# Performance work log

Measured on AMD Instinct MI355X. Metric: run time of the kernel, lower is better.

Reference implementation:

```python
import jax, jax.numpy as jnp
import numpy as np

N_NODES = 100000
DROP_P = 0.1


def gcn_conv(x, W, b, row, col, n_nodes):
    """PyG GCNConv: out = D^{-1/2}(A+I)D^{-1/2} X W + b.
    row/col already include self-loops. Messages flow row(src) -> col(dst)."""
    xw = x @ W  # [N, H]
    deg = jax.ops.segment_sum(jnp.ones_like(col, dtype=xw.dtype), col, num_segments=n_nodes)
    dinv = jnp.where(deg > 0, jax.lax.rsqrt(deg), 0.0)
    norm = dinv[row] * dinv[col]  # [E]
    msg = norm[:, None] * xw[row]  # [E, H] gather + scale
    out = jax.ops.segment_sum(msg, col, num_segments=n_nodes)  # scatter-add
    return out + b


def dropout(x, key, p):
    keep = jax.random.bernoulli(key, 1.0 - p, x.shape)
    return jnp.where(keep, x / (1.0 - p), 0.0).astype(x.dtype)


def prelu(x, alpha):
    return jnp.where(x >= 0, x, alpha[None, :] * x)


def setup_inputs() -> dict:
    key = jax.random.key(0)
    k1, k2, k3, k4 = jax.random.split(key, 4)
    in_ch, hid = 128, 128
    n_edges = 1600000
    x = jax.random.normal(k1, (N_NODES, in_ch), dtype=jnp.float32)
    edge_index = jax.random.randint(k2, (2, n_edges), 0, N_NODES, dtype=jnp.int64)
    s = 1.0 / np.sqrt(in_ch)
    W1 = jax.random.normal(k3, (in_ch, hid), dtype=jnp.float32) * s
    W2 = jax.random.normal(k4, (hid, hid), dtype=jnp.float32) * s
    b1 = jnp.zeros((hid,), dtype=jnp.float32)
    b2 = jnp.zeros((hid,), dtype=jnp.float32)
    alpha = jnp.full((hid,), 0.25, dtype=jnp.float32)
    return {"x": x, "edge_index": edge_index, "W1": W1, "b1": b1,
            "W2": W2, "b2": b2, "alpha": alpha}


def reference(x, edge_index, W1, b1, W2, b2, alpha):
    n = x.shape[0]
    # add self-loops once (PyG default add_self_loops=True)
    loop = jnp.arange(n, dtype=edge_index.dtype)
    row = jnp.concatenate([edge_index[0], loop])
    col = jnp.concatenate([edge_index[1], loop])

    dk1, dk2 = jax.random.split(jax.random.key(42))
    h = gcn_conv(x, W1, b1, row, col, n)
    h = dropout(h, dk1, DROP_P)
    h = prelu(h, alpha)
    h = gcn_conv(h, W2, b2, row, col, n)
    h = dropout(h, dk2, DROP_P)
    h = prelu(h, alpha)
    return h
```

## Files before the change

kernel.cpp:

```cpp
#include <hip/hip_runtime.h>
#include <stdint.h>
#include <string.h>

__host__ __device__ inline uint32_t rotl32(uint32_t x, int r) {
    return (x << r) | (x >> (32 - r));
}

__host__ __device__ inline void tf2x32(uint32_t k0, uint32_t k1,
                                       uint32_t x0, uint32_t x1,
                                       uint32_t& o0, uint32_t& o1) {
    uint32_t ks0 = k0, ks1 = k1, ks2 = k0 ^ k1 ^ 0x1BD11BDAu;
    x0 += ks0; x1 += ks1;
#define TF_R4(a,b,c,d) \
    x0 += x1; x1 = rotl32(x1,a); x1 ^= x0; \
    x0 += x1; x1 = rotl32(x1,b); x1 ^= x0; \
    x0 += x1; x1 = rotl32(x1,c); x1 ^= x0; \
    x0 += x1; x1 = rotl32(x1,d); x1 ^= x0;
    TF_R4(13,15,26,6)  x0 += ks1; x1 += ks2 + 1u;
    TF_R4(17,29,16,24) x0 += ks2; x1 += ks0 + 2u;
    TF_R4(13,15,26,6)  x0 += ks0; x1 += ks1 + 3u;
    TF_R4(17,29,16,24) x0 += ks1; x1 += ks2 + 4u;
    TF_R4(13,15,26,6)  x0 += ks2; x1 += ks0 + 5u;
#undef TF_R4
    o0 = x0; o1 = x1;
}

__device__ inline unsigned pk2h(float a, float b) {
    _Float16 ha = (_Float16)a, hb = (_Float16)b;
    unsigned short ua, ub;
    __builtin_memcpy(&ua, &ha, 2);
    __builtin_memcpy(&ub, &hb, 2);
    return (unsigned)ua | ((unsigned)ub << 16);
}
__device__ inline unsigned short h16bits(float a) {
    _Float16 h = (_Float16)a;
    unsigned short u; __builtin_memcpy(&u, &h, 2);
    return u;
}
__device__ inline float lo16(unsigned u) {
    unsigned short s = (unsigned short)(u & 0xffffu);
    _Float16 h; __builtin_memcpy(&h, &s, 2);
    return (float)h;
}
__device__ inline float hi16(unsigned u) {
    unsigned short s = (unsigned short)(u >> 16);
    _Float16 h; __builtin_memcpy(&h, &s, 2);
    return (float)h;
}

typedef float fx4 __attribute__((ext_vector_type(4)));
typedef unsigned ux4 __attribute__((ext_vector_type(4)));
typedef _Float16 h16x8 __attribute__((ext_vector_type(8)));
typedef float f32x4 __attribute__((ext_vector_type(4)));

#define CSR_CAP 48
#define NSUP 8

__global__ __launch_bounds__(256) void k_build(
        const int* __restrict__ ei, int2* __restrict__ gsup,
        unsigned* __restrict__ gsupcnt,
        unsigned long long* __restrict__ m1, unsigned long long* __restrict__ m2,
        const float* __restrict__ x, unsigned* __restrict__ xb,
        const float* __restrict__ w1, const float* __restrict__ w2,
        _Float16* __restrict__ wt1, _Float16* __restrict__ wt2,
        unsigned k1a, unsigned k1b, unsigned k2a, unsigned k2b,
        int E, int N, int supw, int scap, int total,
        int P1A, int MB, int CB) {
    int b = blockIdx.x;
    int t = (int)threadIdx.x;
    if (b < P1A) {
        __shared__ unsigned hcnt[NSUP], hoff[NSUP], hrun[NSUP];
        if (t < NSUP) { hcnt[t] = 0; hrun[t] = 0; }
        __syncthreads();
        int e0 = b * 2048 + t;
        int r[8], c[8];
        unsigned sp[8];
#pragma unroll
        for (int i = 0; i < 8; i++) {
            int e = e0 + i * 256;
            sp[i] = 0xffu;
            if (e < E) {
                c[i] = __builtin_nontemporal_load(ei + (size_t)E + e);
                r[i] = __builtin_nontemporal_load(ei + e);
                if ((unsigned)c[i] < (unsigned)N && (unsigned)r[i] < (unsigned)N) {
                    sp[i] = (unsigned)c[i] / (unsigned)supw;
                    atomicAdd(&hcnt[sp[i]], 1u);
                }
            }
        }
        __syncthreads();
        if (t < NSUP) hoff[t] = atomicAdd(&gsupcnt[t], hcnt[t]);
        __syncthreads();
#pragma unroll
        for (int i = 0; i < 8; i++) {
            if (sp[i] < (unsigned)NSUP) {
                unsigned rank = atomicAdd(&hrun[sp[i]], 1u);
                unsigned gp = hoff[sp[i]] + rank;
                if (gp < (unsigned)scap)
                    gsup[(size_t)sp[i] * scap + gp] = make_int2(r[i], c[i]);
            }
        }
        return;
    }
    b -= P1A;
    if (b < MB) {
        int wv = (b * 256 + t) >> 6;
        int lane = t & 63;
        int TW = (2 * total) >> 6;
        int half = total >> 6;
        int w0 = wv * 8;
#pragma unroll
        for (int j = 0; j < 8; j++) {
            int wd = w0 + j;
            if (wd < TW) {
                int wl = wd;
                unsigned ka = k1a, kb = k1b;
                unsigned long long* m = m1;
                if (wl >= half) { wl -= half; ka = k2a; kb = k2b; m = m2; }
                uint32_t o0, o1;
                tf2x32(ka, kb, 0u, (uint32_t)(wl * 64 + lane), o0, o1);
                bool keep = (((o0 ^ o1) >> 9) < 7549747u);
                unsigned long long bal = __ballot(keep);
                if (lane == 0)
                    __builtin_nontemporal_store(bal, m + wl);
            }
        }
        return;
    }
    b -= MB;
    if (b < CB) {
        int i = b * 256 + t;
        if (i < (total >> 3)) {
            const fx4* src = (const fx4*)(x + (size_t)i * 8);
            fx4 a = __builtin_nontemporal_load(src);
            fx4 bb = __builtin_nontemporal_load(src + 1);
            ux4 v;
            v.x = pk2h(a.x, a.y);
            v.y = pk2h(a.z, a.w);
            v.z = pk2h(bb.x, bb.y);
            v.w = pk2h(bb.z, bb.w);
            __builtin_nontemporal_store(v, (ux4*)xb + i);
        }
        return;
    }
    b -= CB;
    int idx = b * 256 + t;
    int mat = idx >> 14;
    int e2 = idx & 16383;
    int c = e2 >> 7, k = e2 & 127;
    const float* W = mat ? w2 : w1;
    _Float16* WT = mat ? wt2 : wt1;
    WT[(size_t)c * 128 + k] = (_Float16)W[(size_t)k * 128 + c];
}

__global__ __launch_bounds__(256) void k_fill2(
        const int2* __restrict__ gsup, const unsigned* __restrict__ gsupcnt,
        unsigned* __restrict__ cnt, unsigned* __restrict__ csr, int scap) {
    int s = blockIdx.x & (NSUP - 1);
    int chunk = blockIdx.x >> 3;
    unsigned ne = gsupcnt[s];
    if (ne > (unsigned)scap) ne = (unsigned)scap;
    const int2* base = gsup + (size_t)s * scap;
    unsigned e0 = (unsigned)(chunk * 2048) + threadIdx.x;
#pragma unroll
    for (int i = 0; i < 8; i++) {
        unsigned e = e0 + i * 256;
        if (e < ne) {
            int2 ed = base[e];
            unsigned c = (unsigned)ed.y;
            unsigned slot = atomicAdd(&cnt[c], 1u);
            if (slot < (unsigned)CSR_CAP)
                csr[(size_t)c * CSR_CAP + slot] = (unsigned)ed.x;
        }
    }
}

__global__ void k_dinv(const unsigned* __restrict__ cnt, float* __restrict__ dinv, int N) {
    int n = blockIdx.x * blockDim.x + threadIdx.x;
    if (n >= N) return;
    dinv[n] = rsqrtf((float)cnt[n] + 1.0f);
}

#define UPK_FMA(c, uu)                                   \
    acc[0] = fmaf(c, lo16((uu).x), acc[0]);              \
    acc[1] = fmaf(c, hi16((uu).x), acc[1]);              \
    acc[2] = fmaf(c, lo16((uu).y), acc[2]);              \
    acc[3] = fmaf(c, hi16((uu).y), acc[3]);              \
    acc[4] = fmaf(c, lo16((uu).z), acc[4]);              \
    acc[5] = fmaf(c, hi16((uu).z), acc[5]);              \
    acc[6] = fmaf(c, lo16((uu).w), acc[6]);              \
    acc[7] = fmaf(c, hi16((uu).w), acc[7]);

template <int OUT_HALF>
__global__ __launch_bounds__(256) void k_layer(
        const unsigned short* __restrict__ in,
        const _Float16* __restrict__ WT,
        const float* __restrict__ bias, const float* __restrict__ alpha,
        const unsigned long long* __restrict__ mask,
        const float* __restrict__ dinv, const unsigned* __restrict__ cnt,
        const unsigned* __restrict__ csr,
        void* outv, int n) {
    __shared__ unsigned hl[64 * 68];
    int t = threadIdx.x;
    int rowbase = blockIdx.x * 64;
    int w = t >> 6, l = t & 63;
    int slot = l >> 4;
    int lm = l & 15;
    int ci = lm << 3;

    int prow = rowbase + w * 16 + lm;
    bool pv = prow < n;
    float dnAll = pv ? dinv[prow] : 0.f;
    unsigned cAll = pv ? cnt[prow] : 0u;
    if (cAll > (unsigned)CSR_CAP) cAll = (unsigned)CSR_CAP;

#pragma unroll
    for (int g = 0; g < 4; ++g) {
        int rloc = g * 4 + slot;
        int node = rowbase + w * 16 + rloc;
        float dn = __shfl(dnAll, rloc);
        unsigned ecnt = (unsigned)__shfl((int)cAll, rloc);
        float acc[8];
#pragma unroll
        for (int j = 0; j < 8; j++) acc[j] = 0.f;
        size_t eb = (size_t)node * CSR_CAP;
        unsigned e = 0;
        unsigned nb4 = ecnt >> 2;
#pragma unroll 2
        for (unsigned bb = 0; bb < nb4; ++bb) {
            unsigned r0 = csr[eb + e + 0];
            unsigned r1 = csr[eb + e + 1];
            unsigned r2 = csr[eb + e + 2];
            unsigned r3 = csr[eb + e + 3];
            float c0 = dn * dinv[r0];
            float c1 = dn * dinv[r1];
            float c2 = dn * dinv[r2];
            float c3 = dn * dinv[r3];
            uint4 u0 = *(const uint4*)(in + ((size_t)r0 << 7) + ci);
            uint4 u1 = *(const uint4*)(in + ((size_t)r1 << 7) + ci);
            uint4 u2 = *(const uint4*)(in + ((size_t)r2 << 7) + ci);
            uint4 u3 = *(const uint4*)(in + ((size_t)r3 << 7) + ci);
            UPK_FMA(c0, u0)
            UPK_FMA(c1, u1)
            UPK_FMA(c2, u2)
            UPK_FMA(c3, u3)
            e += 4;
        }
        for (; e < ecnt; ++e) {
            unsigned r0 = csr[eb + e];
            float c0 = dn * dinv[r0];
            uint4 u0 = *(const uint4*)(in + ((size_t)r0 << 7) + ci);
            UPK_FMA(c0, u0)
        }
        if (node < n) {
            uint4 sv = *(const uint4*)(in + ((size_t)node << 7) + ci);
            float dd = dn * dn;
            UPK_FMA(dd, sv)
        }
        uint4 o;
        o.x = pk2h(acc[0], acc[1]);
        o.y = pk2h(acc[2], acc[3]);
        o.z = pk2h(acc[4], acc[5]);
        o.w = pk2h(acc[6], acc[7]);
        *(uint4*)(hl + (size_t)(w * 16 + rloc) * 68 + lm * 4) = o;
    }

    int kq = l >> 4;
    f32x4 facc[8];
#pragma unroll
    for (int f = 0; f < 8; f++) facc[f] = (f32x4){0.f, 0.f, 0.f, 0.f};
#pragma unroll
    for (int kk = 0; kk < 4; kk++) {
        h16x8 a = *(const h16x8*)(hl + (size_t)(w * 16 + lm) * 68 + kq * 4 + kk * 16);
#pragma unroll
        for (int f = 0; f < 8; f++) {
            h16x8 bfr = *(const h16x8*)(WT + (size_t)(f * 16 + lm) * 128 + kk * 32 + kq * 8);
            facc[f] = __builtin_amdgcn_mfma_f32_16x16x32_f16(a, bfr, facc[f], 0, 0, 0);
        }
    }

#pragma unroll
    for (int j = 0; j < 4; j++) {
        int rg = rowbase + w * 16 + kq * 4 + j;
        if (rg < n) {
            unsigned long long wm0 = mask[(size_t)rg << 1];
            unsigned long long wm1 = mask[((size_t)rg << 1) + 1];
#pragma unroll
            for (int f = 0; f < 8; f++) {
                int c = f * 16 + lm;
                float v = facc[f][j] + bias[c];
                unsigned long long wmw = (f < 4) ? wm0 : wm1;
                bool keep = (wmw >> (c & 63)) & 1ull;
                v = keep ? v * (1.0f / 0.9f) : 0.0f;
                float al = alpha[c];
                v = (v >= 0.f) ? v : al * v;
                if (OUT_HALF)
                    ((unsigned short*)outv)[(size_t)rg * 128 + c] = h16bits(v);
                else
                    ((float*)outv)[(size_t)rg * 128 + c] = v;
            }
        }
    }
}

extern "C" void kernel_launch(void* const* d_in, const int* in_sizes, int n_in,
                              void* d_out, int out_size, void* d_ws, size_t ws_size,
                              hipStream_t stream) {
    const float* x  = (const float*)d_in[0];
    const int*   ei = (const int*)d_in[1];
    const float* W1 = (const float*)d_in[2];
    const float* b1 = (const float*)d_in[3];
    const float* W2 = (const float*)d_in[4];
    const float* b2 = (const float*)d_in[5];
    const float* al = (const float*)d_in[6];
    int N = in_sizes[0] / 128;
    int E = in_sizes[1] / 2;
    float* out = (float*)d_out;

    int supw = (N + NSUP - 1) / NSUP;
    int scap = E / NSUP + E / 64 + 4096;

    char* p = (char*)d_ws;
    unsigned short* xb = (unsigned short*)p;   p += (size_t)N * 128 * 2;
    unsigned short* ab = (unsigned short*)p;   p += (size_t)N * 128 * 2;
    int2* gsup = (int2*)ab;
    unsigned* cnt = (unsigned*)p;              p += (size_t)N * 4;
    float* dinv = (float*)p;                   p += (size_t)N * 4;
    unsigned* csr = (unsigned*)p;              p += (size_t)N * CSR_CAP * 4;
    unsigned long long* m1 = (unsigned long long*)p;  p += ((size_t)N * 128 / 64) * 8;
    unsigned long long* m2 = (unsigned long long*)p;  p += ((size_t)N * 128 / 64) * 8;
    _Float16* wt1 = (_Float16*)p;              p += 128 * 128 * 2;
    _Float16* wt2 = (_Float16*)p;              p += 128 * 128 * 2;
    unsigned* gsupcnt = (unsigned*)p;

    hipMemsetAsync(cnt, 0, (size_t)N * 4, stream);
    hipMemsetAsync(gsupcnt, 0, NSUP * 4, stream);

    uint32_t dk1a, dk1b, dk2a, dk2b;
    tf2x32(0u, 42u, 0u, 0u, dk1a, dk1b);
    tf2x32(0u, 42u, 0u, 1u, dk2a, dk2b);

    int total = N * 128;
    int P1A = (E + 2047) / 2048;
    int TW = (2 * total) / 64;
    int MB = (TW + 31) / 32;
    int CB = (total / 8 + 255) / 256;
    int WB = (2 * 128 * 128 + 255) / 256;
    k_build<<<P1A + MB + CB + WB, 256, 0, stream>>>(ei, gsup, gsupcnt, m1, m2,
                                                    x, (unsigned*)xb,
                                                    W1, W2, wt1, wt2,
                                                    dk1a, dk1b, dk2a, dk2b,
                                                    E, N, supw, scap, total,
                                                    P1A, MB, CB);
    int F2C = (scap + 2047) / 2048;
    k_fill2<<<NSUP * F2C, 256, 0, stream>>>(gsup, gsupcnt, cnt, csr, scap);
    k_dinv<<<(N + 255) / 256, 256, 0, stream>>>(cnt, dinv, N);

    int LB = (N + 63) / 64;
    k_layer<1><<<LB, 256, 0, stream>>>(xb, wt1, b1, al, m1, dinv, cnt, csr, ab, N);
    k_layer<0><<<LB, 256, 0, stream>>>(ab, wt2, b2, al, m2, dinv, cnt, csr, out, N);
}
```

Baseline: 371.1 us.

## Prescale features by dinv and accumulate neighbours with packed fp16 adds

The symmetric normalisation is factored so that source rows are prescaled by dinv once, in a new prep kernel for layer 1 and in the layer-1 epilogue for layer 2. The aggregation loop then drops the per-edge dinv gather and multiply and sums neighbours with packed half2 adds, applying the destination dinv once at the end. Layer blocks shrink from four wavefronts to one to raise block count. This removes a random gather per edge and halves the ALU work, but accumulating in fp16 loses precision and risks overflow at high degrees.

```diff
diff --git a/kernel.cpp b/kernel.cpp
--- a/kernel.cpp
+++ b/kernel.cpp
@@ -51,7 +51,10 @@
 typedef float fx4 __attribute__((ext_vector_type(4)));
 typedef unsigned ux4 __attribute__((ext_vector_type(4)));
 typedef _Float16 h16x8 __attribute__((ext_vector_type(8)));
+typedef _Float16 h16x2 __attribute__((ext_vector_type(2)));
 typedef float f32x4 __attribute__((ext_vector_type(4)));
+
+__device__ inline h16x2 as_h2(unsigned u) { h16x2 r; __builtin_memcpy(&r, &u, 4); return r; }
 
 #define CSR_CAP 48
 #define NSUP 8
@@ -175,24 +178,24 @@
     }
 }
 
-__global__ void k_dinv(const unsigned* __restrict__ cnt, float* __restrict__ dinv, int N) {
-    int n = blockIdx.x * blockDim.x + threadIdx.x;
-    if (n >= N) return;
-    dinv[n] = rsqrtf((float)cnt[n] + 1.0f);
-}
-
-#define UPK_FMA(c, uu)                                   \
-    acc[0] = fmaf(c, lo16((uu).x), acc[0]);              \
-    acc[1] = fmaf(c, hi16((uu).x), acc[1]);              \
-    acc[2] = fmaf(c, lo16((uu).y), acc[2]);              \
-    acc[3] = fmaf(c, hi16((uu).y), acc[3]);              \
-    acc[4] = fmaf(c, lo16((uu).z), acc[4]);              \
-    acc[5] = fmaf(c, hi16((uu).z), acc[5]);              \
-    acc[6] = fmaf(c, lo16((uu).w), acc[6]);              \
-    acc[7] = fmaf(c, hi16((uu).w), acc[7]);
+__global__ __launch_bounds__(256) void k_prep(const unsigned* __restrict__ cnt,
+        float* __restrict__ dinv, uint4* __restrict__ xb4, int N) {
+    int i = blockIdx.x * 256 + (int)threadIdx.x;
+    int node = i >> 4, part = i & 15;
+    if (node >= N) return;
+    float d = rsqrtf((float)cnt[node] + 1.0f);
+    if (part == 0) dinv[node] = d;
+    uint4 u = xb4[(size_t)node * 16 + part];
+    uint4 o;
+    o.x = pk2h(d * lo16(u.x), d * hi16(u.x));
+    o.y = pk2h(d * lo16(u.y), d * hi16(u.y));
+    o.z = pk2h(d * lo16(u.z), d * hi16(u.z));
+    o.w = pk2h(d * lo16(u.w), d * hi16(u.w));
+    xb4[(size_t)node * 16 + part] = o;
+}
 
 template <int OUT_HALF>
-__global__ __launch_bounds__(256) void k_layer(
+__global__ __launch_bounds__(64) void k_layer(
         const unsigned short* __restrict__ in,
         const _Float16* __restrict__ WT,
         const float* __restrict__ bias, const float* __restrict__ alpha,
@@ -200,15 +203,14 @@
         const float* __restrict__ dinv, const unsigned* __restrict__ cnt,
         const unsigned* __restrict__ csr,
         void* outv, int n) {
-    __shared__ unsigned hl[64 * 68];
-    int t = threadIdx.x;
-    int rowbase = blockIdx.x * 64;
-    int w = t >> 6, l = t & 63;
+    __shared__ unsigned hl[16 * 68];
+    int l = (int)threadIdx.x;
+    int rowbase = blockIdx.x * 16;
     int slot = l >> 4;
     int lm = l & 15;
     int ci = lm << 3;
 
-    int prow = rowbase + w * 16 + lm;
+    int prow = rowbase + lm;
     bool pv = prow < n;
     float dnAll = pv ? dinv[prow] : 0.f;
     unsigned cAll = pv ? cnt[prow] : 0u;
@@ -217,12 +219,10 @@
 #pragma unroll
     for (int g = 0; g < 4; ++g) {
         int rloc = g * 4 + slot;
-        int node = rowbase + w * 16 + rloc;
+        int node = rowbase + rloc;
         float dn = __shfl(dnAll, rloc);
         unsigned ecnt = (unsigned)__shfl((int)cAll, rloc);
-        float acc[8];
-#pragma unroll
-        for (int j = 0; j < 8; j++) acc[j] = 0.f;
+        h16x2 a0 = (h16x2)0, a1 = (h16x2)0, a2 = (h16x2)0, a3 = (h16x2)0;
         size_t eb = (size_t)node * CSR_CAP;
         unsigned e = 0;
         unsigned nb4 = ecnt >> 2;
@@ -232,37 +232,31 @@
             unsigned r1 = csr[eb + e + 1];
             unsigned r2 = csr[eb + e + 2];
             unsigned r3 = csr[eb + e + 3];
-            float c0 = dn * dinv[r0];
-            float c1 = dn * dinv[r1];
-            float c2 = dn * dinv[r2];
-            float c3 = dn * dinv[r3];
             uint4 u0 = *(const uint4*)(in + ((size_t)r0 << 7) + ci);
             uint4 u1 = *(const uint4*)(in + ((size_t)r1 << 7) + ci);
             uint4 u2 = *(const uint4*)(in + ((size_t)r2 << 7) + ci);
             uint4 u3 = *(const uint4*)(in + ((size_t)r3 << 7) + ci);
-            UPK_FMA(c0, u0)
-            UPK_FMA(c1, u1)
-            UPK_FMA(c2, u2)
-            UPK_FMA(c3, u3)
+            a0 += as_h2(u0.x); a1 += as_h2(u0.y); a2 += as_h2(u0.z); a3 += as_h2(u0.w);
+            a0 += as_h2(u1.x); a1 += as_h2(u1.y); a2 += as_h2(u1.z); a3 += as_h2(u1.w);
+            a0 += as_h2(u2.x); a1 += as_h2(u2.y); a2 += as_h2(u2.z); a3 += as_h2(u2.w);
+            a0 += as_h2(u3.x); a1 += as_h2(u3.y); a2 += as_h2(u3.z); a3 += as_h2(u3.w);
             e += 4;
         }
         for (; e < ecnt; ++e) {
             unsigned r0 = csr[eb + e];
-            float c0 = dn * dinv[r0];
             uint4 u0 = *(const uint4*)(in + ((size_t)r0 << 7) + ci);
-            UPK_FMA(c0, u0)
+            a0 += as_h2(u0.x); a1 += as_h2(u0.y); a2 += as_h2(u0.z); a3 += as_h2(u0.w);
         }
         if (node < n) {
             uint4 sv = *(const uint4*)(in + ((size_t)node << 7) + ci);
-            float dd = dn * dn;
-            UPK_FMA(dd, sv)
+            a0 += as_h2(sv.x); a1 += as_h2(sv.y); a2 += as_h2(sv.z); a3 += as_h2(sv.w);
         }
         uint4 o;
-        o.x = pk2h(acc[0], acc[1]);
-        o.y = pk2h(acc[2], acc[3]);
-        o.z = pk2h(acc[4], acc[5]);
-        o.w = pk2h(acc[6], acc[7]);
-        *(uint4*)(hl + (size_t)(w * 16 + rloc) * 68 + lm * 4) = o;
+        o.x = pk2h(dn * (float)a0[0], dn * (float)a0[1]);
+        o.y = pk2h(dn * (float)a1[0], dn * (float)a1[1]);
+        o.z = pk2h(dn * (float)a2[0], dn * (float)a2[1]);
+        o.w = pk2h(dn * (float)a3[0], dn * (float)a3[1]);
+        *(uint4*)(hl + (size_t)rloc * 68 + lm * 4) = o;
     }
 
     int kq = l >> 4;
@@ -271,7 +265,7 @@
     for (int f = 0; f < 8; f++) facc[f] = (f32x4){0.f, 0.f, 0.f, 0.f};
 #pragma unroll
     for (int kk = 0; kk < 4; kk++) {
-        h16x8 a = *(const h16x8*)(hl + (size_t)(w * 16 + lm) * 68 + kq * 4 + kk * 16);
+        h16x8 a = *(const h16x8*)(hl + (size_t)lm * 68 + kq * 4 + kk * 16);
 #pragma unroll
         for (int f = 0; f < 8; f++) {
             h16x8 bfr = *(const h16x8*)(WT + (size_t)(f * 16 + lm) * 128 + kk * 32 + kq * 8);
@@ -281,8 +275,10 @@
 
 #pragma unroll
     for (int j = 0; j < 4; j++) {
-        int rg = rowbase + w * 16 + kq * 4 + j;
+        int rl = kq * 4 + j;
+        int rg = rowbase + rl;
         if (rg < n) {
+            float dnrow = __shfl(dnAll, rl);
             unsigned long long wm0 = mask[(size_t)rg << 1];
             unsigned long long wm1 = mask[((size_t)rg << 1) + 1];
 #pragma unroll
@@ -295,7 +291,7 @@
                 float al = alpha[c];
                 v = (v >= 0.f) ? v : al * v;
                 if (OUT_HALF)
-                    ((unsigned short*)outv)[(size_t)rg * 128 + c] = h16bits(v);
+                    ((unsigned short*)outv)[(size_t)rg * 128 + c] = h16bits(v * dnrow);
                 else
                     ((float*)outv)[(size_t)rg * 128 + c] = v;
             }
@@ -354,9 +350,9 @@
                                                     P1A, MB, CB);
     int F2C = (scap + 2047) / 2048;
     k_fill2<<<NSUP * F2C, 256, 0, stream>>>(gsup, gsupcnt, cnt, csr, scap);
-    k_dinv<<<(N + 255) / 256, 256, 0, stream>>>(cnt, dinv, N);
-
-    int LB = (N + 63) / 64;
-    k_layer<1><<<LB, 256, 0, stream>>>(xb, wt1, b1, al, m1, dinv, cnt, csr, ab, N);
-    k_layer<0><<<LB, 256, 0, stream>>>(ab, wt2, b2, al, m2, dinv, cnt, csr, out, N);
-}
+    k_prep<<<(N * 16 + 255) / 256, 256, 0, stream>>>(cnt, dinv, (uint4*)xb, N);
+
+    int LB = (N + 15) / 16;
+    k_layer<1><<<LB, 64, 0, stream>>>(xb, wt1, b1, al, m1, dinv, cnt, csr, ab, N);
+    k_layer<0><<<LB, 64, 0, stream>>>(ab, wt2, b2, al, m2, dinv, cnt, csr, out, N);
+}
```

Result: faster. 353.2 us (-4.8%).
